# Optimization experiments

Measured on AMD Instinct MI355X. Metric: run time of the kernel, lower is better.

The kernel has to match this reference:

```python
import jax, jax.numpy as jnp
import numpy as np

D_MODEL = 1024
NUM_EXPERTS = 64
TOP_K = 2
TEMPERATURE = 1.0


def setup_inputs() -> dict:
    key = jax.random.key(0)
    k1, k2, k3, k4 = jax.random.split(key, 4)
    mh_output = jax.random.normal(k1, (8, 4096, D_MODEL), dtype=jnp.float32)
    noise = jax.random.normal(k2, (8, 4096, NUM_EXPERTS), dtype=jnp.float32)  # randn_like sample, externalized
    # nn.Linear weights: shape [out, in], init normal(0, 0.02); biases zero
    W_route = jax.random.normal(k3, (NUM_EXPERTS, D_MODEL), dtype=jnp.float32) * 0.02
    b_route = jnp.zeros((NUM_EXPERTS,), dtype=jnp.float32)
    W_noise = jax.random.normal(k4, (NUM_EXPERTS, D_MODEL), dtype=jnp.float32) * 0.02
    b_noise = jnp.zeros((NUM_EXPERTS,), dtype=jnp.float32)
    return {"mh_output": mh_output, "noise": noise, "W_route": W_route,
            "b_route": b_route, "W_noise": W_noise, "b_noise": b_noise}


def reference(mh_output, noise, W_route, b_route, W_noise, b_noise):
    # logits = topkroute_linear(mh_output); noise_logits = noise_linear(mh_output)
    logits = jnp.einsum('bsd,ed->bse', mh_output, W_route) + b_route
    noise_logits = jnp.einsum('bsd,ed->bse', mh_output, W_noise) + b_noise
    # noisy logits = logits + temperature * randn * softplus(noise_logits)
    noisy = logits + TEMPERATURE * noise * jax.nn.softplus(noise_logits)
    # top-k, scatter into -inf, softmax  ==  softmax over top-k values scattered into zeros
    top_vals, indices = jax.lax.top_k(noisy, TOP_K)          # [b, s, k]
    probs_k = jax.nn.softmax(top_vals, axis=-1)              # softmax(-inf elsewhere) -> 0 elsewhere
    one_hot = jax.nn.one_hot(indices, NUM_EXPERTS, dtype=noisy.dtype)  # [b, s, k, E]
    router_output = jnp.sum(one_hot * probs_k[..., None], axis=-2)     # [b, s, E]
    return router_output, indices
```

## Files before the change

### kernel.cpp

```cpp
#include <hip/hip_runtime.h>
#include <hip/hip_bf16.h>
#include <math.h>


#define T_TOKENS 32768
#define D_MODEL  1024
#define NE       64
#define NCOL     128
#define M_TILE   64
#define KSTAGE   64
#define NSTAGE   16
#define CS_LD    68
#define OUT_IDX_BASE ((size_t)T_TOKENS * NE)
#define W_ELEMS  (NCOL * D_MODEL)

typedef short  bf16x8  __attribute__((ext_vector_type(8)));
typedef float  floatx4 __attribute__((ext_vector_type(4)));

__device__ __forceinline__ float softplus_f(float x) {
    return fmaxf(x, 0.f) + log1pf(expf(-fabsf(x)));
}

__device__ __forceinline__ void cvt8(const float4 a, const float4 b,
                                     int4* hi, int4* lo) {
    float v[8] = {a.x, a.y, a.z, a.w, b.x, b.y, b.z, b.w};
    int hw[4], lw[4];
    #pragma unroll
    for (int p = 0; p < 4; ++p) {
        float2 f2 = make_float2(v[2 * p], v[2 * p + 1]);
        __hip_bfloat162 h2 = __float22bfloat162_rn(f2);
        int u; __builtin_memcpy(&u, &h2, 4);
        float h0 = __uint_as_float(((unsigned)u) << 16);
        float h1 = __uint_as_float(((unsigned)u) & 0xFFFF0000u);
        float2 l2 = make_float2(v[2 * p] - h0, v[2 * p + 1] - h1);
        __hip_bfloat162 L2 = __float22bfloat162_rn(l2);
        int ul; __builtin_memcpy(&ul, &L2, 4);
        hw[p] = u; lw[p] = ul;
    }
    *hi = make_int4(hw[0], hw[1], hw[2], hw[3]);
    *lo = make_int4(lw[0], lw[1], lw[2], lw[3]);
}

__global__ __launch_bounds__(256) void prepack_w(
    const float* __restrict__ Wr, const float* __restrict__ Wn,
    short* __restrict__ Bh, short* __restrict__ Bl)
{
    int g   = blockIdx.x * 256 + threadIdx.x;
    int n   = g & 15;
    int kg  = (g >> 4) & 127;
    int t2  = g >> 11;
    int col = t2 * 16 + n;
    const float* src = (col < NE ? Wr + (size_t)col * D_MODEL
                                 : Wn + (size_t)(col - NE) * D_MODEL) + kg * 8;
    float4 a = *(const float4*)src;
    float4 b = *(const float4*)(src + 4);
    int4 hi, lo;
    cvt8(a, b, &hi, &lo);
    *(int4*)(Bh + (size_t)g * 8) = hi;
    *(int4*)(Bl + (size_t)g * 8) = lo;
}

__global__ __launch_bounds__(256, 2) void router_mfma(
    const float* __restrict__ A,
    const float* __restrict__ noise,
    const float* __restrict__ br,
    const float* __restrict__ bn,
    const short* __restrict__ Bh,
    const short* __restrict__ Bl,
    float* __restrict__ out)
{
    __shared__ __align__(16) short Ah[2][M_TILE * KSTAGE];
    __shared__ __align__(16) short Al[2][M_TILE * KSTAGE];
    __shared__ float Cs[M_TILE * CS_LD];
    __shared__ float s_p1[M_TILE], s_p2[M_TILE];
    __shared__ int   s_e1[M_TILE], s_e2[M_TILE];

    const int tid  = threadIdx.x;
    const int lane = tid & 63;
    const int wid  = tid >> 6;
    const int n16  = lane & 15;
    const int quad = lane >> 4;
    const int m0   = blockIdx.x * M_TILE;

    const int r  = tid & 63;
    const int g  = tid >> 6;
    const float* pA = A + (size_t)(m0 + r) * D_MODEL + g * 8;
    const int sBase = (g * M_TILE + r) * 8;

    const short* pBhR = Bh + ((size_t)(wid * 128 + quad) * 16 + n16) * 8;
    const short* pBlR = Bl + ((size_t)(wid * 128 + quad) * 16 + n16) * 8;
    const short* pBhN = Bh + ((size_t)((4 + wid) * 128 + quad) * 16 + n16) * 8;
    const short* pBlN = Bl + ((size_t)((4 + wid) * 128 + quad) * 16 + n16) * 8;

    floatx4 acc[4][2];
    #pragma unroll
    for (int i = 0; i < 4; ++i) { acc[i][0] = (floatx4)0.f; acc[i][1] = (floatx4)0.f; }

    {
        float4 a0 = *(const float4*)(pA);
        float4 a1 = *(const float4*)(pA + 4);
        float4 a2 = *(const float4*)(pA + 32);
        float4 a3 = *(const float4*)(pA + 36);
        int4 hi, lo;
        cvt8(a0, a1, &hi, &lo);
        *(int4*)&Ah[0][sBase] = hi;
        *(int4*)&Al[0][sBase] = lo;
        cvt8(a2, a3, &hi, &lo);
        *(int4*)&Ah[0][sBase + 2048] = hi;
        *(int4*)&Al[0][sBase + 2048] = lo;
    }
    float4 nx0a = *(const float4*)(pA + KSTAGE);
    float4 nx0b = *(const float4*)(pA + KSTAGE + 4);
    float4 nx1a = *(const float4*)(pA + KSTAGE + 32);
    float4 nx1b = *(const float4*)(pA + KSTAGE + 36);
    bf16x8 c0hR = *(const bf16x8*)(pBhR);
    bf16x8 c0lR = *(const bf16x8*)(pBlR);
    bf16x8 c0hN = *(const bf16x8*)(pBhN);
    bf16x8 c0lN = *(const bf16x8*)(pBlN);
    __syncthreads();

    float nz[4][4];

    #pragma unroll 2
    for (int s = 0; s < NSTAGE; ++s) {
        const int cur = s & 1, nxt = cur ^ 1;

        float4 f0a, f0b, f1a, f1b;
        if (s + 2 < NSTAGE) {
            const float* q = pA + (s + 2) * KSTAGE;
            f0a = *(const float4*)(q);
            f0b = *(const float4*)(q + 4);
            f1a = *(const float4*)(q + 32);
            f1b = *(const float4*)(q + 36);
        }

        const int ob1 = (s * 2 + 1) * 512;
        bf16x8 c1hR = *(const bf16x8*)(pBhR + ob1);
        bf16x8 c1lR = *(const bf16x8*)(pBlR + ob1);
        bf16x8 c1hN = *(const bf16x8*)(pBhN + ob1);
        bf16x8 c1lN = *(const bf16x8*)(pBlN + ob1);
        bf16x8 n0hR, n0lR, n0hN, n0lN;
        if (s + 1 < NSTAGE) {
            const int ob0 = (s + 1) * 2 * 512;
            n0hR = *(const bf16x8*)(pBhR + ob0);
            n0lR = *(const bf16x8*)(pBlR + ob0);
            n0hN = *(const bf16x8*)(pBhN + ob0);
            n0lN = *(const bf16x8*)(pBlN + ob0);
        }

        if (s == NSTAGE - 3) {
            const int e = wid * 16 + n16;
            #pragma unroll
            for (int mf = 0; mf < 4; ++mf)
                #pragma unroll
                for (int rr = 0; rr < 4; ++rr)
                    nz[mf][rr] = noise[(size_t)(m0 + mf * 16 + quad * 4 + rr) * NE + e];
        }

        #pragma unroll
        for (int mf = 0; mf < 4; ++mf) {
            const int gi = (quad * M_TILE + mf * 16 + n16) * 8;
            bf16x8 afh = *(const bf16x8*)&Ah[cur][gi];
            bf16x8 afl = *(const bf16x8*)&Al[cur][gi];
            acc[mf][0] = __builtin_amdgcn_mfma_f32_16x16x32_bf16(afh, c0hR, acc[mf][0], 0, 0, 0);
            acc[mf][0] = __builtin_amdgcn_mfma_f32_16x16x32_bf16(afh, c0lR, acc[mf][0], 0, 0, 0);
            acc[mf][0] = __builtin_amdgcn_mfma_f32_16x16x32_bf16(afl, c0hR, acc[mf][0], 0, 0, 0);
            acc[mf][1] = __builtin_amdgcn_mfma_f32_16x16x32_bf16(afh, c0hN, acc[mf][1], 0, 0, 0);
            acc[mf][1] = __builtin_amdgcn_mfma_f32_16x16x32_bf16(afh, c0lN, acc[mf][1], 0, 0, 0);
            acc[mf][1] = __builtin_amdgcn_mfma_f32_16x16x32_bf16(afl, c0hN, acc[mf][1], 0, 0, 0);
        }
        #pragma unroll
        for (int mf = 0; mf < 4; ++mf) {
            const int gi = ((4 + quad) * M_TILE + mf * 16 + n16) * 8;
            bf16x8 afh = *(const bf16x8*)&Ah[cur][gi];
            bf16x8 afl = *(const bf16x8*)&Al[cur][gi];
            acc[mf][0] = __builtin_amdgcn_mfma_f32_16x16x32_bf16(afh, c1hR, acc[mf][0], 0, 0, 0);
            acc[mf][0] = __builtin_amdgcn_mfma_f32_16x16x32_bf16(afh, c1lR, acc[mf][0], 0, 0, 0);
            acc[mf][0] = __builtin_amdgcn_mfma_f32_16x16x32_bf16(afl, c1hR, acc[mf][0], 0, 0, 0);
            acc[mf][1] = __builtin_amdgcn_mfma_f32_16x16x32_bf16(afh, c1hN, acc[mf][1], 0, 0, 0);
            acc[mf][1] = __builtin_amdgcn_mfma_f32_16x16x32_bf16(afh, c1lN, acc[mf][1], 0, 0, 0);
            acc[mf][1] = __builtin_amdgcn_mfma_f32_16x16x32_bf16(afl, c1hN, acc[mf][1], 0, 0, 0);
        }

        if (s + 1 < NSTAGE) {
            int4 hi, lo;
            cvt8(nx0a, nx0b, &hi, &lo);
            *(int4*)&Ah[nxt][sBase] = hi;
            *(int4*)&Al[nxt][sBase] = lo;
            cvt8(nx1a, nx1b, &hi, &lo);
            *(int4*)&Ah[nxt][sBase + 2048] = hi;
            *(int4*)&Al[nxt][sBase + 2048] = lo;
        }

        __syncthreads();

        nx0a = f0a; nx0b = f0b; nx1a = f1a; nx1b = f1b;
        c0hR = n0hR; c0lR = n0lR; c0hN = n0hN; c0lN = n0lN;
    }

    {
        const int e = wid * 16 + n16;
        float brv = br[e], bnv = bn[e];
        #pragma unroll
        for (int mf = 0; mf < 4; ++mf)
            #pragma unroll
            for (int rr = 0; rr < 4; ++rr) {
                int t = mf * 16 + quad * 4 + rr;
                float route = acc[mf][0][rr] + brv;
                float nl    = acc[mf][1][rr] + bnv;
                Cs[t * CS_LD + e] = fmaf(nz[mf][rr], softplus_f(nl), route);
            }
    }
    __syncthreads();

    if (lane < 16) {
        const int t = wid * 16 + lane;
        float v1 = -INFINITY, v2 = -INFINITY;
        int e1 = 0, e2 = 0;
        #pragma unroll
        for (int e4 = 0; e4 < 16; ++e4) {
            float4 q = *(const float4*)&Cs[t * CS_LD + e4 * 4];
            float qa[4] = {q.x, q.y, q.z, q.w};
            #pragma unroll
            for (int c = 0; c < 4; ++c) {
                float v = qa[c];
                int e = e4 * 4 + c;
                if (v > v1) { v2 = v1; e2 = e1; v1 = v; e1 = e; }
                else if (v > v2) { v2 = v; e2 = e; }
            }
        }
        float ex = expf(v2 - v1);
        float denom = 1.f + ex;
        s_p1[t] = 1.f / denom;
        s_p2[t] = ex / denom;
        s_e1[t] = e1;
        s_e2[t] = e2;
        float2 iv = make_float2((float)e1, (float)e2);
        *(float2*)(out + OUT_IDX_BASE + (size_t)(m0 + t) * 2) = iv;
    }
    __syncthreads();

    #pragma unroll
    for (int i = 0; i < 4; ++i) {
        int gi = i * 256 + tid;
        int t  = gi >> 4;
        int e0 = (gi & 15) * 4;
        float p1 = s_p1[t], p2 = s_p2[t];
        int   e1 = s_e1[t], e2 = s_e2[t];
        float4 v;
        v.x = (e0 + 0 == e1) ? p1 : ((e0 + 0 == e2) ? p2 : 0.f);
        v.y = (e0 + 1 == e1) ? p1 : ((e0 + 1 == e2) ? p2 : 0.f);
        v.z = (e0 + 2 == e1) ? p1 : ((e0 + 2 == e2) ? p2 : 0.f);
        v.w = (e0 + 3 == e1) ? p1 : ((e0 + 3 == e2) ? p2 : 0.f);
        *(float4*)(out + (size_t)(m0 + t) * NE + e0) = v;
    }
}

extern "C" void kernel_launch(void* const* d_in, const int* in_sizes, int n_in,
                              void* d_out, int out_size, void* d_ws, size_t ws_size,
                              hipStream_t stream) {
    const float* A     = (const float*)d_in[0];
    const float* noise = (const float*)d_in[1];
    const float* Wr    = (const float*)d_in[2];
    const float* br    = (const float*)d_in[3];
    const float* Wn    = (const float*)d_in[4];
    const float* bn    = (const float*)d_in[5];
    float* out = (float*)d_out;

    short* Bh = (short*)d_ws;
    short* Bl = Bh + W_ELEMS;

    prepack_w<<<dim3(W_ELEMS / 8 / 256), dim3(256), 0, stream>>>(Wr, Wn, Bh, Bl);
    router_mfma<<<dim3(T_TOKENS / M_TILE), dim3(256), 0, stream>>>(A, noise, br, bn, Bh, Bl, out);
}
```

Measured before the change: 230.1 us.

## Double K-stage depth, alias epilogue buffer onto A tiles, stagger K start per block

Doubles the K-stage width to 128 and halves the stage count, so each sync covers twice as much MFMA work. The epilogue buffer Cs now aliases the A staging shared memory, which offsets the larger A tiles and keeps two blocks per CU possible. Each group of 8 blocks also starts the K loop at a different phase, spreading weight and activation reads across different address ranges to reduce channel or cache contention. The cost is higher register pressure from holding four prefetched float4 pairs and four sets of B fragments, which may cause spills or lower occupancy.

```diff
diff --git a/kernel.cpp b/kernel.cpp
--- a/kernel.cpp
+++ b/kernel.cpp
@@ -8,8 +8,8 @@
 #define NE       64
 #define NCOL     128
 #define M_TILE   64
-#define KSTAGE   64
-#define NSTAGE   16
+#define KSTAGE   128
+#define NSTAGE   8
 #define CS_LD    68
 #define OUT_IDX_BASE ((size_t)T_TOKENS * NE)
 #define W_ELEMS  (NCOL * D_MODEL)
@@ -71,9 +71,9 @@
 {
     __shared__ __align__(16) short Ah[2][M_TILE * KSTAGE];
     __shared__ __align__(16) short Al[2][M_TILE * KSTAGE];
-    __shared__ float Cs[M_TILE * CS_LD];
     __shared__ float s_p1[M_TILE], s_p2[M_TILE];
     __shared__ int   s_e1[M_TILE], s_e2[M_TILE];
+    float* Cs = reinterpret_cast<float*>(&Ah[0][0]);
 
     const int tid  = threadIdx.x;
     const int lane = tid & 63;
@@ -82,6 +82,8 @@
     const int quad = lane >> 4;
     const int m0   = blockIdx.x * M_TILE;
 
+    const int phase = (blockIdx.x >> 3) & (NSTAGE - 1);
+
     const int r  = tid & 63;
     const int g  = tid >> 6;
     const float* pA = A + (size_t)(m0 + r) * D_MODEL + g * 8;
@@ -96,56 +98,68 @@
     #pragma unroll
     for (int i = 0; i < 4; ++i) { acc[i][0] = (floatx4)0.f; acc[i][1] = (floatx4)0.f; }
 
+    const int w0 = phase;
+    const int w1 = (phase + 1) & (NSTAGE - 1);
     {
-        float4 a0 = *(const float4*)(pA);
-        float4 a1 = *(const float4*)(pA + 4);
-        float4 a2 = *(const float4*)(pA + 32);
-        float4 a3 = *(const float4*)(pA + 36);
-        int4 hi, lo;
-        cvt8(a0, a1, &hi, &lo);
-        *(int4*)&Ah[0][sBase] = hi;
-        *(int4*)&Al[0][sBase] = lo;
-        cvt8(a2, a3, &hi, &lo);
-        *(int4*)&Ah[0][sBase + 2048] = hi;
-        *(int4*)&Al[0][sBase + 2048] = lo;
-    }
-    float4 nx0a = *(const float4*)(pA + KSTAGE);
-    float4 nx0b = *(const float4*)(pA + KSTAGE + 4);
-    float4 nx1a = *(const float4*)(pA + KSTAGE + 32);
-    float4 nx1b = *(const float4*)(pA + KSTAGE + 36);
-    bf16x8 c0hR = *(const bf16x8*)(pBhR);
-    bf16x8 c0lR = *(const bf16x8*)(pBlR);
-    bf16x8 c0hN = *(const bf16x8*)(pBhN);
-    bf16x8 c0lN = *(const bf16x8*)(pBlN);
+        const float* q = pA + w0 * KSTAGE;
+        #pragma unroll
+        for (int c = 0; c < 4; ++c) {
+            float4 a0 = *(const float4*)(q + c * 32);
+            float4 a1 = *(const float4*)(q + c * 32 + 4);
+            int4 hi, lo;
+            cvt8(a0, a1, &hi, &lo);
+            *(int4*)&Ah[0][sBase + c * 2048] = hi;
+            *(int4*)&Al[0][sBase + c * 2048] = lo;
+        }
+    }
+    float4 nxa[4], nxb[4];
+    {
+        const float* q = pA + w1 * KSTAGE;
+        #pragma unroll
+        for (int c = 0; c < 4; ++c) {
+            nxa[c] = *(const float4*)(q + c * 32);
+            nxb[c] = *(const float4*)(q + c * 32 + 4);
+        }
+    }
+    bf16x8 c0hR = *(const bf16x8*)(pBhR + (w0 * 4) * 512);
+    bf16x8 c0lR = *(const bf16x8*)(pBlR + (w0 * 4) * 512);
+    bf16x8 c0hN = *(const bf16x8*)(pBhN + (w0 * 4) * 512);
+    bf16x8 c0lN = *(const bf16x8*)(pBlN + (w0 * 4) * 512);
     __syncthreads();
 
     float nz[4][4];
 
-    #pragma unroll 2
     for (int s = 0; s < NSTAGE; ++s) {
         const int cur = s & 1, nxt = cur ^ 1;
-
-        float4 f0a, f0b, f1a, f1b;
+        const int ps  = (s + phase) & (NSTAGE - 1);
+
+        float4 fa[4], fb[4];
         if (s + 2 < NSTAGE) {
-            const float* q = pA + (s + 2) * KSTAGE;
-            f0a = *(const float4*)(q);
-            f0b = *(const float4*)(q + 4);
-            f1a = *(const float4*)(q + 32);
-            f1b = *(const float4*)(q + 36);
-        }
-
-        const int ob1 = (s * 2 + 1) * 512;
-        bf16x8 c1hR = *(const bf16x8*)(pBhR + ob1);
-        bf16x8 c1lR = *(const bf16x8*)(pBlR + ob1);
-        bf16x8 c1hN = *(const bf16x8*)(pBhN + ob1);
-        bf16x8 c1lN = *(const bf16x8*)(pBlN + ob1);
+            const float* q = pA + ((ps + 2) & (NSTAGE - 1)) * KSTAGE;
+            #pragma unroll
+            for (int c = 0; c < 4; ++c) {
+                fa[c] = *(const float4*)(q + c * 32);
+                fb[c] = *(const float4*)(q + c * 32 + 4);
+            }
+        }
+
+        bf16x8 bh[4][2], bl[4][2];
+        bh[0][0] = c0hR; bl[0][0] = c0lR; bh[0][1] = c0hN; bl[0][1] = c0lN;
+        #pragma unroll
+        for (int c = 1; c < 4; ++c) {
+            const int o = (ps * 4 + c) * 512;
+            bh[c][0] = *(const bf16x8*)(pBhR + o);
+            bl[c][0] = *(const bf16x8*)(pBlR + o);
+            bh[c][1] = *(const bf16x8*)(pBhN + o);
+            bl[c][1] = *(const bf16x8*)(pBlN + o);
+        }
         bf16x8 n0hR, n0lR, n0hN, n0lN;
         if (s + 1 < NSTAGE) {
-            const int ob0 = (s + 1) * 2 * 512;
-            n0hR = *(const bf16x8*)(pBhR + ob0);
-            n0lR = *(const bf16x8*)(pBlR + ob0);
-            n0hN = *(const bf16x8*)(pBhN + ob0);
-            n0lN = *(const bf16x8*)(pBlN + ob0);
+            const int o = (((ps + 1) & (NSTAGE - 1)) * 4) * 512;
+            n0hR = *(const bf16x8*)(pBhR + o);
+            n0lR = *(const bf16x8*)(pBlR + o);
+            n0hN = *(const bf16x8*)(pBhN + o);
+            n0lN = *(const bf16x8*)(pBlN + o);
         }
 
         if (s == NSTAGE - 3) {
@@ -158,43 +172,35 @@
         }
 
         #pragma unroll
-        for (int mf = 0; mf < 4; ++mf) {
-            const int gi = (quad * M_TILE + mf * 16 + n16) * 8;
-            bf16x8 afh = *(const bf16x8*)&Ah[cur][gi];
-            bf16x8 afl = *(const bf16x8*)&Al[cur][gi];
-            acc[mf][0] = __builtin_amdgcn_mfma_f32_16x16x32_bf16(afh, c0hR, acc[mf][0], 0, 0, 0);
-            acc[mf][0] = __builtin_amdgcn_mfma_f32_16x16x32_bf16(afh, c0lR, acc[mf][0], 0, 0, 0);
-            acc[mf][0] = __builtin_amdgcn_mfma_f32_16x16x32_bf16(afl, c0hR, acc[mf][0], 0, 0, 0);
-            acc[mf][1] = __builtin_amdgcn_mfma_f32_16x16x32_bf16(afh, c0hN, acc[mf][1], 0, 0, 0);
-            acc[mf][1] = __builtin_amdgcn_mfma_f32_16x16x32_bf16(afh, c0lN, acc[mf][1], 0, 0, 0);
-            acc[mf][1] = __builtin_amdgcn_mfma_f32_16x16x32_bf16(afl, c0hN, acc[mf][1], 0, 0, 0);
-        }
-        #pragma unroll
-        for (int mf = 0; mf < 4; ++mf) {
-            const int gi = ((4 + quad) * M_TILE + mf * 16 + n16) * 8;
-            bf16x8 afh = *(const bf16x8*)&Ah[cur][gi];
-            bf16x8 afl = *(const bf16x8*)&Al[cur][gi];
-            acc[mf][0] = __builtin_amdgcn_mfma_f32_16x16x32_bf16(afh, c1hR, acc[mf][0], 0, 0, 0);
-            acc[mf][0] = __builtin_amdgcn_mfma_f32_16x16x32_bf16(afh, c1lR, acc[mf][0], 0, 0, 0);
-            acc[mf][0] = __builtin_amdgcn_mfma_f32_16x16x32_bf16(afl, c1hR, acc[mf][0], 0, 0, 0);
-            acc[mf][1] = __builtin_amdgcn_mfma_f32_16x16x32_bf16(afh, c1hN, acc[mf][1], 0, 0, 0);
-            acc[mf][1] = __builtin_amdgcn_mfma_f32_16x16x32_bf16(afh, c1lN, acc[mf][1], 0, 0, 0);
-            acc[mf][1] = __builtin_amdgcn_mfma_f32_16x16x32_bf16(afl, c1hN, acc[mf][1], 0, 0, 0);
+        for (int c = 0; c < 4; ++c) {
+            #pragma unroll
+            for (int mf = 0; mf < 4; ++mf) {
+                const int gi = ((c * 4 + quad) * M_TILE + mf * 16 + n16) * 8;
+                bf16x8 afh = *(const bf16x8*)&Ah[cur][gi];
+                bf16x8 afl = *(const bf16x8*)&Al[cur][gi];
+                acc[mf][0] = __builtin_amdgcn_mfma_f32_16x16x32_bf16(afh, bh[c][0], acc[mf][0], 0, 0, 0);
+                acc[mf][0] = __builtin_amdgcn_mfma_f32_16x16x32_bf16(afh, bl[c][0], acc[mf][0], 0, 0, 0);
+                acc[mf][0] = __builtin_amdgcn_mfma_f32_16x16x32_bf16(afl, bh[c][0], acc[mf][0], 0, 0, 0);
+                acc[mf][1] = __builtin_amdgcn_mfma_f32_16x16x32_bf16(afh, bh[c][1], acc[mf][1], 0, 0, 0);
+                acc[mf][1] = __builtin_amdgcn_mfma_f32_16x16x32_bf16(afh, bl[c][1], acc[mf][1], 0, 0, 0);
+                acc[mf][1] = __builtin_amdgcn_mfma_f32_16x16x32_bf16(afl, bh[c][1], acc[mf][1], 0, 0, 0);
+            }
         }
 
         if (s + 1 < NSTAGE) {
-            int4 hi, lo;
-            cvt8(nx0a, nx0b, &hi, &lo);
-            *(int4*)&Ah[nxt][sBase] = hi;
-            *(int4*)&Al[nxt][sBase] = lo;
-            cvt8(nx1a, nx1b, &hi, &lo);
-            *(int4*)&Ah[nxt][sBase + 2048] = hi;
-            *(int4*)&Al[nxt][sBase + 2048] = lo;
+            #pragma unroll
+            for (int c = 0; c < 4; ++c) {
+                int4 hi, lo;
+                cvt8(nxa[c], nxb[c], &hi, &lo);
+                *(int4*)&Ah[nxt][sBase + c * 2048] = hi;
+                *(int4*)&Al[nxt][sBase + c * 2048] = lo;
+            }
         }
 
         __syncthreads();
 
-        nx0a = f0a; nx0b = f0b; nx1a = f1a; nx1b = f1b;
+        #pragma unroll
+        for (int c = 0; c < 4; ++c) { nxa[c] = fa[c]; nxb[c] = fb[c]; }
         c0hR = n0hR; c0lR = n0lR; c0hN = n0hN; c0lN = n0lN;
     }
 
```

New measurement: 227.9 us. About the same (-1.0%).
